# Optimization experiments

Hardware: AMD Instinct MI355X
Metric: run time of the kernel (lower is better)

Reference implementation:

```python
import jax, jax.numpy as jnp
import numpy as np

B, T, F, H, P = 4, 1024, 500, 128, 64


def setup_inputs() -> dict:
    key = jax.random.key(0)
    ks = jax.random.split(key, 10)
    s_gru = 1.0 / np.sqrt(H)
    s_ctx = 1.0 / np.sqrt(2 * H * P)
    s_fc = 1.0 / np.sqrt(H)
    return {
        "x": jax.random.normal(ks[0], (B, T, F), dtype=jnp.float32),
        "W_ih": jax.random.uniform(ks[1], (3 * H, F), jnp.float32, -s_gru, s_gru),
        "W_hh": jax.random.uniform(ks[2], (3 * H, H), jnp.float32, -s_gru, s_gru),
        "b_ih": jax.random.uniform(ks[3], (3 * H,), jnp.float32, -s_gru, s_gru),
        "b_hh": jax.random.uniform(ks[4], (3 * H,), jnp.float32, -s_gru, s_gru),
        "W_ctx": jax.random.uniform(ks[5], (H, 2 * H * P), jnp.float32, -s_ctx, s_ctx),
        "b_ctx": jax.random.uniform(ks[6], (H,), jnp.float32, -s_ctx, s_ctx),
        "W_fc": jax.random.uniform(ks[7], (P, H), jnp.float32, -s_fc, s_fc),
        "b_fc": jax.random.uniform(ks[8], (P,), jnp.float32, -s_fc, s_fc),
    }


def reference(x, W_ih, W_hh, b_ih, b_hh, W_ctx, b_ctx, W_fc, b_fc):
    # Original torch code never updates `hidden` inside the time loop, so every
    # GRU step runs with h = 0 (W_hh contributes only through b_hh). For a
    # 1-layer GRU, output == new state. PyTorch gate order: r, z, n.
    Bv, Tv, _ = x.shape
    Hv = W_hh.shape[1]
    Pv = W_fc.shape[0]
    gi = jnp.einsum('btf,gf->btg', x, W_ih) + b_ih          # [B,T,3H]
    gr, gz, gn = jnp.split(gi, 3, axis=-1)
    br, bz, bn = jnp.split(b_hh, 3)
    r = jax.nn.sigmoid(gr + br)
    z = jax.nn.sigmoid(gz + bz)
    n = jnp.tanh(gn + r * bn)                               # W_hh @ 0 == 0
    states = (1.0 - z) * n                                  # [B,T,H], h' = (1-z)*n + z*0
    all_states = jnp.transpose(states, (1, 0, 2))           # [T,B,H]

    # context_mat[:, :, j] at step i = concat(state_i, state_{max(i-j,0)})
    idx = jnp.clip(jnp.arange(Tv)[:, None] - jnp.arange(Pv)[None, :], 0)  # [T,P]
    gathered = all_states[idx]                              # [T,P,B,H]
    part1 = jnp.broadcast_to(all_states[:, :, :, None], (Tv, Bv, Hv, Pv))
    part2 = jnp.transpose(gathered, (0, 2, 3, 1))           # [T,B,H,P]
    # flatten matches torch .view(B, -1) of [B, 2H, P]: channel-major then proposal
    ctx_in = jnp.concatenate([part1, part2], axis=2).reshape(Tv, Bv, 2 * Hv * Pv)
    gate = jax.nn.sigmoid(jnp.einsum('tbc,hc->tbh', ctx_in, W_ctx) + b_ctx)
    gated = all_states * gate                               # output_i * ctx gate

    outs = jnp.transpose(gated, (1, 0, 2))                  # [B,T,H]
    probs = jax.nn.sigmoid(jnp.einsum('bth,ph->btp', outs, W_fc) + b_fc)
    probs = jnp.clip(probs, 0.001, 0.999)                   # [B,T,P]
    return probs, all_states
```

## Files before the change

kernel.cpp:

```cpp
#include <hip/hip_runtime.h>


typedef short bf16x8 __attribute__((ext_vector_type(8)));
typedef float f32x4 __attribute__((ext_vector_type(4)));
typedef float f32x16 __attribute__((ext_vector_type(16)));
typedef unsigned short u16;
typedef unsigned int u32;

__device__ __forceinline__ float bf2f(u16 u) {
  union { u32 i; float f; } v; v.i = ((u32)u) << 16; return v.f;
}
__device__ __forceinline__ u16 f2bf(float f) {
  union { float f; u32 i; } v; v.f = f;
  u32 u = v.i;
  return (u16)((u + 0x7FFFu + ((u >> 16) & 1u)) >> 16);
}
__device__ __forceinline__ u32 pack2(float a, float b) {
  return (u32)f2bf(a) | ((u32)f2bf(b) << 16);
}
__device__ __forceinline__ float sigmoidf_(float x) {
  return 1.0f / (1.0f + __expf(-x));
}

__global__ __launch_bounds__(512, 4) void k_front(const float* __restrict__ x,
                                                  const float* __restrict__ W_ih,
                                                  u16* __restrict__ gi_bf,
                                                  const float* __restrict__ W_ctx,
                                                  u16* __restrict__ WcT) {
  __shared__ __align__(16) char smem[49152];
  const int tid = threadIdx.x;
  const int bid = blockIdx.x;

  if (bid < 192) {
    typedef u16 AsmT[64][64];
    typedef u16 BsmT[128][64];
    AsmT* Asm = (AsmT*)smem;
    BsmT* Bsm = (BsmT*)(smem + 16384);
    const int w = tid >> 6, lane = tid & 63;
    const int l15 = lane & 15, quad = lane >> 4;
    const int wm = (w & 1) * 32, wn = (w >> 1) * 32;
    const int m0 = (bid & 63) * 64;
    const int n0 = (bid >> 6) * 128;
    f32x4 acc[2][2];
    for (int i = 0; i < 2; ++i)
      for (int j = 0; j < 2; ++j) acc[i][j] = (f32x4){0.f, 0.f, 0.f, 0.f};

    uint4 ra, rb[2];
    auto cvt_load = [](const float* base, int k) -> uint4 {
      float4 a = make_float4(0.f, 0.f, 0.f, 0.f), b = a;
      if (k < 500)     a = *(const float4*)(base + k);
      if (k + 4 < 500) b = *(const float4*)(base + k + 4);
      uint4 o; o.x = pack2(a.x, a.y); o.y = pack2(a.z, a.w);
      o.z = pack2(b.x, b.y); o.w = pack2(b.z, b.w);
      return o;
    };
    auto load_step = [&](int s) {
      int kc = s * 64;
      {
        int c = tid;
        ra = cvt_load(x + (size_t)(m0 + (c >> 3)) * 500, kc + (c & 7) * 8);
      }
#pragma unroll
      for (int j = 0; j < 2; ++j) {
        int c = j * 512 + tid;
        rb[j] = cvt_load(W_ih + (size_t)(n0 + (c >> 3)) * 500, kc + (c & 7) * 8);
      }
    };
    auto write_step = [&](int b) {
      {
        int c = tid;
        int r = c >> 3, pc = (c & 7) ^ (r & 7);
        *(uint4*)&Asm[b][r][pc * 8] = ra;
      }
#pragma unroll
      for (int j = 0; j < 2; ++j) {
        int c = j * 512 + tid;
        int r = c >> 3, pc = (c & 7) ^ (r & 7);
        *(uint4*)&Bsm[b][r][pc * 8] = rb[j];
      }
    };

    load_step(0); write_step(0); __syncthreads();
    for (int s = 0; s < 8; ++s) {
      int cur = s & 1;
      if (s < 7) load_step(s + 1);
#pragma unroll
      for (int kk = 0; kk < 2; ++kk) {
        int ch = kk * 4 + quad;
        bf16x8 af[2], bfr[2];
#pragma unroll
        for (int mt = 0; mt < 2; ++mt) {
          int r = wm + mt * 16 + l15;
          af[mt] = *(const bf16x8*)&Asm[cur][r][(ch ^ (r & 7)) * 8];
        }
#pragma unroll
        for (int nt = 0; nt < 2; ++nt) {
          int r = wn + nt * 16 + l15;
          bfr[nt] = *(const bf16x8*)&Bsm[cur][r][(ch ^ (r & 7)) * 8];
        }
#pragma unroll
        for (int mt = 0; mt < 2; ++mt)
#pragma unroll
          for (int nt = 0; nt < 2; ++nt)
            acc[mt][nt] = __builtin_amdgcn_mfma_f32_16x16x32_bf16(af[mt], bfr[nt], acc[mt][nt], 0, 0, 0);
      }
      if (s < 7) write_step((s + 1) & 1);
      __syncthreads();
    }
    for (int mt = 0; mt < 2; ++mt)
      for (int nt = 0; nt < 2; ++nt)
        for (int rg = 0; rg < 4; ++rg) {
          int m = m0 + wm + mt * 16 + quad * 4 + rg;
          int n = n0 + wn + nt * 16 + l15;
          gi_bf[m * 384 + n] = f2bf(acc[mt][nt][rg]);
        }
  } else {
    typedef float T2Row[68];
    T2Row* t2 = (T2Row*)smem;
    float* s1 = (float*)(smem + 34816);
    const int hp = bid - 192;
    const float* wrow = W_ctx + hp * 16384;
    for (int it = 0; it < 4; ++it) {
      int i = it * 512 + tid;
      int j = i * 4;
      int h = j >> 6, q = j & 63;
      *(float4*)&t2[h][q] = *(const float4*)(wrow + 8192 + j);
    }
    {
      const int w = tid >> 6, lane = tid & 63;
      for (int rr = w; rr < 128; rr += 8) {
        float v = wrow[rr * 64 + lane];
#pragma unroll
        for (int off = 32; off; off >>= 1) v += __shfl_down(v, off, 64);
        if (lane == 0) s1[rr] = v;
      }
    }
    __syncthreads();
    for (int it = 0; it < 4; ++it) {
      int i = it * 512 + tid;
      int p = i >> 5, h0 = (i & 31) * 4;
      float v0 = t2[h0 + 0][p], v1 = t2[h0 + 1][p];
      float v2 = t2[h0 + 2][p], v3 = t2[h0 + 3][p];
      if (p == 0) { v0 += s1[h0]; v1 += s1[h0 + 1]; v2 += s1[h0 + 2]; v3 += s1[h0 + 3]; }
      uint2 o; o.x = pack2(v0, v1); o.y = pack2(v2, v3);
      *(uint2*)(WcT + ((size_t)(p * 16 + (h0 >> 3)) * 128 + hp) * 8 + (h0 & 7)) = o;
    }
  }
}

__global__ void k_states(const u16* __restrict__ gi_bf,
                         const float* __restrict__ b_ih, const float* __restrict__ b_hh,
                         u16* __restrict__ S_bf, float* __restrict__ out_states) {
  int g = blockIdx.x * 256 + threadIdx.x;
  int r = g >> 5, h0 = (g & 31) * 4;
  const u16* gr = gi_bf + r * 384;
  uint2 ur = *(const uint2*)(gr + h0);
  uint2 uz = *(const uint2*)(gr + 128 + h0);
  uint2 un = *(const uint2*)(gr + 256 + h0);
  float4 bir = *(const float4*)(b_ih + h0);
  float4 biz = *(const float4*)(b_ih + 128 + h0);
  float4 bin = *(const float4*)(b_ih + 256 + h0);
  float4 bhr = *(const float4*)(b_hh + h0);
  float4 bhz = *(const float4*)(b_hh + 128 + h0);
  float4 bhn = *(const float4*)(b_hh + 256 + h0);
  float xr[4] = { bf2f((u16)ur.x) + bir.x + bhr.x, bf2f((u16)(ur.x >> 16)) + bir.y + bhr.y,
                  bf2f((u16)ur.y) + bir.z + bhr.z, bf2f((u16)(ur.y >> 16)) + bir.w + bhr.w };
  float xz[4] = { bf2f((u16)uz.x) + biz.x + bhz.x, bf2f((u16)(uz.x >> 16)) + biz.y + bhz.y,
                  bf2f((u16)uz.y) + biz.z + bhz.z, bf2f((u16)(uz.y >> 16)) + biz.w + bhz.w };
  float xn[4] = { bf2f((u16)un.x) + bin.x, bf2f((u16)(un.x >> 16)) + bin.y,
                  bf2f((u16)un.y) + bin.z, bf2f((u16)(un.y >> 16)) + bin.w };
  float bn[4] = { bhn.x, bhn.y, bhn.z, bhn.w };
  float s[4];
#pragma unroll
  for (int j = 0; j < 4; ++j) {
    float rg = sigmoidf_(xr[j]);
    float zg = sigmoidf_(xz[j]);
    float n = tanhf(xn[j] + rg * bn[j]);
    s[j] = (1.f - zg) * n;
  }
  int b = r >> 10, t = r & 1023;
  size_t o = (size_t)(t * 4 + b) * 128 + h0;
  uint2 sb; sb.x = pack2(s[0], s[1]); sb.y = pack2(s[2], s[3]);
  *(uint2*)(S_bf + o) = sb;
  float4 so = make_float4(s[0], s[1], s[2], s[3]);
  *(float4*)(out_states + o) = so;
}

__global__ __launch_bounds__(128, 2) void k_gemm_ctx(const u16* __restrict__ S_bf,
                                                     const u16* __restrict__ WcT,
                                                     float* __restrict__ partial) {
  __shared__ u16 Awin[92][128];
  const int tid = threadIdx.x;
  const int w = tid >> 6, lane = tid & 63;
  const int l31 = lane & 31, half = lane >> 5;
  const int wn = w * 64;
  const int m0 = blockIdx.x * 64;
  const int P0 = blockIdx.y * 8;
  const int tlo = (m0 >> 2) - P0 - 7;
  f32x16 acc[2][2];
#pragma unroll
  for (int i = 0; i < 16; ++i) {
    acc[0][0][i] = 0.f; acc[0][1][i] = 0.f;
    acc[1][0][i] = 0.f; acc[1][1][i] = 0.f;
  }

  for (int it = 0; it < 12; ++it) {
    int idx = it * 128 + tid;
    if (idx < 1472) {
      int r = idx >> 4, ch = idx & 15;
      int t = tlo + (r >> 2); if (t < 0) t = 0;
      uint4 v = *(const uint4*)(S_bf + (size_t)(t * 4 + (r & 3)) * 128 + ch * 8);
      *(uint4*)&Awin[r][((ch ^ (r & 15)) & 15) * 8] = v;
    }
  }
  __syncthreads();

  const u16* wbase = WcT + (size_t)half * 1024 + (size_t)(wn + l31) * 8;
#pragma unroll
  for (int pi = 0; pi < 8; ++pi) {
    const int shift = 4 * (7 - pi);
    const u16* wp = wbase + (size_t)((P0 + pi) * 16) * 1024;
#pragma unroll
    for (int ks = 0; ks < 8; ++ks) {
      bf16x8 bfr[2];
      bfr[0] = *(const bf16x8*)(wp + (size_t)(ks * 2) * 1024);
      bfr[1] = *(const bf16x8*)(wp + (size_t)(ks * 2) * 1024 + 256);
      int kc = ks * 2 + half;
      bf16x8 af[2];
#pragma unroll
      for (int mt = 0; mt < 2; ++mt) {
        int r = mt * 32 + shift + l31;
        af[mt] = *(const bf16x8*)&Awin[r][((kc ^ (r & 15)) & 15) * 8];
      }
#pragma unroll
      for (int mt = 0; mt < 2; ++mt)
#pragma unroll
        for (int nt = 0; nt < 2; ++nt)
          acc[mt][nt] = __builtin_amdgcn_mfma_f32_32x32x16_bf16(af[mt], bfr[nt], acc[mt][nt], 0, 0, 0);
    }
  }
  float* op = partial + (size_t)blockIdx.y * 524288;
#pragma unroll
  for (int mt = 0; mt < 2; ++mt)
#pragma unroll
    for (int nt = 0; nt < 2; ++nt)
#pragma unroll
      for (int rg = 0; rg < 16; ++rg) {
        int m = m0 + mt * 32 + (rg & 3) + 8 * (rg >> 2) + 4 * half;
        int n = wn + nt * 32 + l31;
        op[m * 128 + n] = acc[mt][nt][rg];
      }
}

__global__ __launch_bounds__(256) void k_epilogue(const float* __restrict__ partial,
                                                  const float* __restrict__ states,
                                                  const float* __restrict__ b_ctx,
                                                  const float* __restrict__ W_fc,
                                                  const float* __restrict__ b_fc,
                                                  float* __restrict__ out_probs) {
  __shared__ float Wfc2[64][128];
  __shared__ float gated[16][128];
  const int tid = threadIdx.x;
  const int row0 = blockIdx.x * 16;
  for (int it = 0; it < 8; ++it) {
    int i = it * 256 + tid;
    int pp = i >> 5, c = i & 31;
    float4 v = *(const float4*)(W_fc + i * 4);
    *(float4*)&Wfc2[pp][((c ^ pp) & 31) * 4] = v;
  }
  for (int it = 0; it < 2; ++it) {
    int i = it * 256 + tid;
    int lr = i >> 5, h0 = (i & 31) * 4;
    int sr = row0 + lr;
    float4 gp = *(const float4*)(b_ctx + h0);
#pragma unroll
    for (int c = 0; c < 8; ++c) {
      float4 pv = *(const float4*)(partial + (size_t)c * 524288 + (size_t)sr * 128 + h0);
      gp.x += pv.x; gp.y += pv.y; gp.z += pv.z; gp.w += pv.w;
    }
    float4 st = *(const float4*)(states + (size_t)sr * 128 + h0);
    float4 gv;
    gv.x = st.x * sigmoidf_(gp.x);
    gv.y = st.y * sigmoidf_(gp.y);
    gv.z = st.z * sigmoidf_(gp.z);
    gv.w = st.w * sigmoidf_(gp.w);
    *(float4*)&gated[lr][h0] = gv;
  }
  __syncthreads();
  for (int it = 0; it < 4; ++it) {
    int o = it * 256 + tid;
    int lr = o >> 6, pp = o & 63;
    int sr = row0 + lr;
    float dot = 0.f;
#pragma unroll
    for (int i = 0; i < 32; ++i) {
      float4 g = *(const float4*)&gated[lr][i * 4];
      float4 wv = *(const float4*)&Wfc2[pp][((i ^ pp) & 31) * 4];
      dot += g.x * wv.x + g.y * wv.y + g.z * wv.z + g.w * wv.w;
    }
    float pv = sigmoidf_(dot + b_fc[pp]);
    pv = (pv > 0.001f) ? pv : 0.001f;
    pv = (pv < 0.999f) ? pv : 0.999f;
    int t = sr >> 2, b = sr & 3;
    out_probs[(b * 1024 + t) * 64 + pp] = pv;
  }
}

extern "C" void kernel_launch(void* const* d_in, const int* in_sizes, int n_in,
                              void* d_out, int out_size, void* d_ws, size_t ws_size,
                              hipStream_t stream) {
  const float* x     = (const float*)d_in[0];
  const float* W_ih  = (const float*)d_in[1];
  const float* b_ih  = (const float*)d_in[3];
  const float* b_hh  = (const float*)d_in[4];
  const float* W_ctx = (const float*)d_in[5];
  const float* b_ctx = (const float*)d_in[6];
  const float* W_fc  = (const float*)d_in[7];
  const float* b_fc  = (const float*)d_in[8];
  float* out = (float*)d_out;

  char* ws = (char*)d_ws;
  u16*   gi_bf   = (u16*)  (ws + 0);
  u16*   S_bf    = (u16*)  (ws + 3145728);
  u16*   WcT     = (u16*)  (ws + 4194304);
  float* partial = (float*)(ws + 6291456);

  k_front<<<320, 512, 0, stream>>>(x, W_ih, gi_bf, W_ctx, WcT);
  k_states<<<512, 256, 0, stream>>>(gi_bf, b_ih, b_hh, S_bf, out + 262144);
  k_gemm_ctx<<<dim3(64, 8), 128, 0, stream>>>(S_bf, WcT, partial);
  k_epilogue<<<256, 256, 0, stream>>>(partial, out + 262144, b_ctx, W_fc, b_fc, out);
}
```

Baseline: 129.6 us.

## Split ctx GEMM K-loop across two wave pairs with LDS reduction

Doubles the k_gemm_ctx block to 256 threads and splits each block's 8 proposal slices between two wave pairs, so each wave does 4 instead of 8 K-iterations. The two partial accumulators are combined through a shared-memory buffer that reuses the A-window LDS before the global store. This shortens per-wave serial MFMA chains and raises wave count per CU. The cost is extra barriers, LDS traffic for the reduction, and more threads per block under the same launch bound.

```diff
diff --git a/kernel.cpp b/kernel.cpp
--- a/kernel.cpp
+++ b/kernel.cpp
@@ -186,14 +186,17 @@
   *(float4*)(out_states + o) = so;
 }
 
-__global__ __launch_bounds__(128, 2) void k_gemm_ctx(const u16* __restrict__ S_bf,
+__global__ __launch_bounds__(256, 2) void k_gemm_ctx(const u16* __restrict__ S_bf,
                                                      const u16* __restrict__ WcT,
                                                      float* __restrict__ partial) {
-  __shared__ u16 Awin[92][128];
+  __shared__ __align__(16) char smem[32768];
+  u16 (*Awin)[128] = (u16(*)[128])smem;
+  float (*S2)[64][64] = (float(*)[64][64])smem;
   const int tid = threadIdx.x;
   const int w = tid >> 6, lane = tid & 63;
   const int l31 = lane & 31, half = lane >> 5;
-  const int wn = w * 64;
+  const int ph = w & 1;
+  const int nh = w >> 1;
   const int m0 = blockIdx.x * 64;
   const int P0 = blockIdx.y * 8;
   const int tlo = (m0 >> 2) - P0 - 7;
@@ -204,8 +207,8 @@
     acc[1][0][i] = 0.f; acc[1][1][i] = 0.f;
   }
 
-  for (int it = 0; it < 12; ++it) {
-    int idx = it * 128 + tid;
+  for (int it = 0; it < 6; ++it) {
+    int idx = it * 256 + tid;
     if (idx < 1472) {
       int r = idx >> 4, ch = idx & 15;
       int t = tlo + (r >> 2); if (t < 0) t = 0;
@@ -215,9 +218,10 @@
   }
   __syncthreads();
 
-  const u16* wbase = WcT + (size_t)half * 1024 + (size_t)(wn + l31) * 8;
-#pragma unroll
-  for (int pi = 0; pi < 8; ++pi) {
+  const u16* wbase = WcT + (size_t)half * 1024 + (size_t)(nh * 64 + l31) * 8;
+#pragma unroll
+  for (int pj = 0; pj < 4; ++pj) {
+    const int pi = ph * 4 + pj;
     const int shift = 4 * (7 - pi);
     const u16* wp = wbase + (size_t)((P0 + pi) * 16) * 1024;
 #pragma unroll
@@ -239,17 +243,33 @@
           acc[mt][nt] = __builtin_amdgcn_mfma_f32_32x32x16_bf16(af[mt], bfr[nt], acc[mt][nt], 0, 0, 0);
     }
   }
-  float* op = partial + (size_t)blockIdx.y * 524288;
-#pragma unroll
-  for (int mt = 0; mt < 2; ++mt)
-#pragma unroll
-    for (int nt = 0; nt < 2; ++nt)
-#pragma unroll
-      for (int rg = 0; rg < 16; ++rg) {
-        int m = m0 + mt * 32 + (rg & 3) + 8 * (rg >> 2) + 4 * half;
-        int n = wn + nt * 32 + l31;
-        op[m * 128 + n] = acc[mt][nt][rg];
-      }
+
+  __syncthreads();
+  if (ph == 0) {
+#pragma unroll
+    for (int mt = 0; mt < 2; ++mt)
+#pragma unroll
+      for (int nt = 0; nt < 2; ++nt)
+#pragma unroll
+        for (int rg = 0; rg < 16; ++rg) {
+          int m = mt * 32 + (rg & 3) + 8 * (rg >> 2) + 4 * half;
+          S2[nh][m][nt * 32 + l31] = acc[mt][nt][rg];
+        }
+  }
+  __syncthreads();
+  if (ph == 1) {
+    float* op = partial + (size_t)blockIdx.y * 524288;
+#pragma unroll
+    for (int mt = 0; mt < 2; ++mt)
+#pragma unroll
+      for (int nt = 0; nt < 2; ++nt)
+#pragma unroll
+        for (int rg = 0; rg < 16; ++rg) {
+          int m = mt * 32 + (rg & 3) + 8 * (rg >> 2) + 4 * half;
+          int n = nh * 64 + nt * 32 + l31;
+          op[(size_t)(m0 + m) * 128 + n] = acc[mt][nt][rg] + S2[nh][m][nt * 32 + l31];
+        }
+  }
 }
 
 __global__ __launch_bounds__(256) void k_epilogue(const float* __restrict__ partial,
@@ -327,6 +347,6 @@
 
   k_front<<<320, 512, 0, stream>>>(x, W_ih, gi_bf, W_ctx, WcT);
   k_states<<<512, 256, 0, stream>>>(gi_bf, b_ih, b_hh, S_bf, out + 262144);
-  k_gemm_ctx<<<dim3(64, 8), 128, 0, stream>>>(S_bf, WcT, partial);
+  k_gemm_ctx<<<dim3(64, 8), 256, 0, stream>>>(S_bf, WcT, partial);
   k_epilogue<<<256, 256, 0, stream>>>(partial, out + 262144, b_ctx, W_fc, b_fc, out);
 }
```

Result: faster. 120.7 us (-6.9%).
